# Optimization experiments

Measured on AMD Instinct MI355X. Metric: run time of the kernel, lower is better.

Reference implementation:

```python
import jax, jax.numpy as jnp
import numpy as np

D_MODEL = 1024
NUM_HEADS = 16
HEAD_DIM = D_MODEL // NUM_HEADS


def setup_inputs() -> dict:
    key = jax.random.key(0)
    k1, k2, k3 = jax.random.split(key, 3)
    B, S = 2, 2048
    x = jax.random.normal(k1, (B, S, D_MODEL), dtype=jnp.float32)
    # torch nn.Linear weight layout: [out_features, in_features]
    qkv_w = jax.random.normal(k2, (3 * D_MODEL, D_MODEL), dtype=jnp.float32) * (D_MODEL ** -0.5)
    qkv_b = jnp.zeros((3 * D_MODEL,), dtype=jnp.float32)
    out_w = jax.random.normal(k3, (D_MODEL, D_MODEL), dtype=jnp.float32) * (D_MODEL ** -0.5)
    out_b = jnp.zeros((D_MODEL,), dtype=jnp.float32)
    return {"x": x, "qkv_w": qkv_w, "qkv_b": qkv_b, "out_w": out_w, "out_b": out_b}


def reference(x, qkv_w, qkv_b, out_w, out_b):
    B, S, D = x.shape
    H, hd = NUM_HEADS, HEAD_DIM
    # fused QKV projection (torch Linear: x @ W.T + b)
    qkv = jnp.dot(x, qkv_w.T) + qkv_b              # [B, S, 3D]
    qkv = qkv.reshape(B, S, 3, H, hd)
    qkv = jnp.transpose(qkv, (2, 0, 3, 1, 4))       # [3, B, H, S, hd]
    q, k, v = qkv[0], qkv[1], qkv[2]
    scale = hd ** -0.5
    scores = jnp.einsum('bhqd,bhkd->bhqk', q, k) * scale  # [B, H, S, S]
    # causal mask (TritonSoftmax(is_causal=True))
    causal = jnp.tril(jnp.ones((S, S), dtype=bool))
    scores = jnp.where(causal, scores, jnp.float32(-jnp.inf))
    attn = jax.nn.softmax(scores, axis=-1)
    ctx = jnp.einsum('bhqk,bhkd->bhqd', attn, v)    # [B, H, S, hd]
    ctx = jnp.transpose(ctx, (0, 2, 1, 3)).reshape(B, S, D)
    return jnp.dot(ctx, out_w.T) + out_b
```

## Files before the change

kernel.cpp:

```cpp
#include <hip/hip_runtime.h>

typedef unsigned short u16;
typedef __bf16 bf16x8 __attribute__((ext_vector_type(8)));
typedef float f32x4 __attribute__((ext_vector_type(4)));

#define LOG2E 1.44269504088896340736f

__device__ __forceinline__ u16 f2bf(float f) {
  unsigned int u = __builtin_bit_cast(unsigned int, f);
  u += 0x7FFFu + ((u >> 16) & 1u);
  return (u16)(u >> 16);
}

__device__ __forceinline__ void async16(const void* g, void* l) {
  __builtin_amdgcn_global_load_lds((void*)g, (void*)l, 16, 0, 0);
}

__global__ void cast_f32_bf16(const float* __restrict__ src, u16* __restrict__ dst, int n4) {
  int i = blockIdx.x * blockDim.x + threadIdx.x;
  if (i >= n4) return;
  float4 v = ((const float4*)src)[i];
  union { u16 s[4]; uint2 u; } o;
  o.s[0] = f2bf(v.x); o.s[1] = f2bf(v.y); o.s[2] = f2bf(v.z); o.s[3] = f2bf(v.w);
  ((uint2*)dst)[i] = o.u;
}

template <int EPI>
__global__ __launch_bounds__(256)
void gemm_nt(const u16* __restrict__ A, const u16* __restrict__ Bw,
             int M, int N, int K, const float* __restrict__ bias,
             u16* __restrict__ qo, u16* __restrict__ ko, u16* __restrict__ vto,
             float* __restrict__ out, int ntn) {
  __shared__ __align__(16) u16 As[128 * 32];
  __shared__ __align__(16) u16 Bs[128 * 32];
  const int tid = threadIdx.x;
  const int w = tid >> 6, lane = tid & 63;
  const int lr = lane & 15, lkb = lane >> 4;
  const int bx = blockIdx.x;
  const int mt = bx / ntn, nt = bx % ntn;
  const int m0 = mt * 128, n0 = nt * 128;
  const int wm = (w >> 1) * 64, wn = (w & 1) * 64;

  f32x4 acc[4][4] = {};

  int srow[2], sgch[2];
#pragma unroll
  for (int i = 0; i < 2; ++i) {
    int cid = tid + i * 256;
    srow[i] = cid >> 2;
    sgch[i] = (cid & 3) ^ (srow[i] & 3);
  }

  for (int k0 = 0; k0 < K; k0 += 32) {
#pragma unroll
    for (int i = 0; i < 2; ++i) {
      char* la = (char*)As + (w * 64 + i * 256) * 16;
      async16(A + (size_t)(m0 + srow[i]) * K + k0 + sgch[i] * 8, la);
      char* lb = (char*)Bs + (w * 64 + i * 256) * 16;
      async16(Bw + (size_t)(n0 + srow[i]) * K + k0 + sgch[i] * 8, lb);
    }
    __syncthreads();

    bf16x8 af[4], bfr[4];
#pragma unroll
    for (int i = 0; i < 4; ++i) {
      int ra = wm + i * 16 + lr;
      af[i] = *(const bf16x8*)(As + ra * 32 + (lkb ^ (ra & 3)) * 8);
      int rb = wn + i * 16 + lr;
      bfr[i] = *(const bf16x8*)(Bs + rb * 32 + (lkb ^ (rb & 3)) * 8);
    }
#pragma unroll
    for (int i = 0; i < 4; ++i)
#pragma unroll
      for (int j = 0; j < 4; ++j)
        acc[i][j] = __builtin_amdgcn_mfma_f32_16x16x32_bf16(af[i], bfr[j], acc[i][j], 0, 0, 0);
    __syncthreads();
  }

  if constexpr (EPI == 0) {
    const int which = n0 >> 10;
    const float qscale = (which == 0) ? 0.125f : 1.0f;
#pragma unroll
    for (int i = 0; i < 4; ++i) {
#pragma unroll
      for (int j = 0; j < 4; ++j) {
        int n = n0 + wn + j * 16 + lr;
        float bv = bias[n];
        int d = n & 1023, h = d >> 6, dd = d & 63;
#pragma unroll
        for (int r = 0; r < 4; ++r) {
          int m = m0 + wm + i * 16 + lkb * 4 + r;
          int b = m >> 11, s = m & 2047;
          int bh = b * 16 + h;
          u16 val = f2bf((acc[i][j][r] + bv) * qscale);
          if (which == 0)      qo[(bh * 2048 + s) * 64 + dd] = val;
          else if (which == 1) ko[(bh * 2048 + s) * 64 + dd] = val;
          else                 vto[(bh * 64 + dd) * 2048 + s] = val;
        }
      }
    }
  } else {
#pragma unroll
    for (int i = 0; i < 4; ++i)
#pragma unroll
      for (int j = 0; j < 4; ++j) {
        int n = n0 + wn + j * 16 + lr;
        float bv = bias[n];
#pragma unroll
        for (int r = 0; r < 4; ++r) {
          int m = m0 + wm + i * 16 + lkb * 4 + r;
          out[(size_t)m * N + n] = acc[i][j][r] + bv;
        }
      }
  }
}

__global__ __launch_bounds__(256)
void flash_attn(const u16* __restrict__ Q, const u16* __restrict__ Kg,
                const u16* __restrict__ Vt, u16* __restrict__ ctx) {
  __shared__ __align__(16) u16 Kls[64 * 64];
  __shared__ __align__(16) u16 Vls[64 * 64];
  __shared__ __align__(16) u16 Pls[4][16 * 72];
  const int tid = threadIdx.x;
  const int w = tid >> 6, lane = tid & 63;
  const int lr = lane & 15, lkb = lane >> 4;
  const int bid = blockIdx.x;
  const int qt = 31 - (bid >> 5);
  const int bh = bid & 31;
  const int q0 = qt * 64;
  const u16* Qh = Q + (size_t)bh * 2048 * 64;
  const u16* Kh = Kg + (size_t)bh * 2048 * 64;
  const u16* Vh = Vt + (size_t)bh * 2048 * 64;

  bf16x8 aQ[2];
#pragma unroll
  for (int kk = 0; kk < 2; ++kk)
    aQ[kk] = *(const bf16x8*)(Qh + (q0 + w * 16 + lr) * 64 + lkb * 8 + kk * 32);

  f32x4 acc[4] = {};
  float mrow[4] = {-1e30f, -1e30f, -1e30f, -1e30f};
  float lrow[4] = {0.f, 0.f, 0.f, 0.f};

  int srow[2], sgch[2];
#pragma unroll
  for (int i = 0; i < 2; ++i) {
    int cid = tid + i * 256;
    srow[i] = cid >> 3;
    sgch[i] = (cid & 7) ^ (srow[i] & 7);
  }

  const int nkv = qt + 1;
  for (int t = 0; t < nkv; ++t) {
    const int kv0 = t * 64;
#pragma unroll
    for (int i = 0; i < 2; ++i) {
      char* lk = (char*)Kls + (w * 64 + i * 256) * 16;
      async16(Kh + (size_t)(kv0 + srow[i]) * 64 + sgch[i] * 8, lk);
      char* lv = (char*)Vls + (w * 64 + i * 256) * 16;
      async16(Vh + (size_t)srow[i] * 2048 + kv0 + sgch[i] * 8, lv);
    }
    __syncthreads();

    f32x4 sc[4];
#pragma unroll
    for (int ct = 0; ct < 4; ++ct) {
      int row = ct * 16 + lr;
      int rs = row & 7;
      bf16x8 b0 = *(const bf16x8*)(Kls + row * 64 + (lkb ^ rs) * 8);
      bf16x8 b1 = *(const bf16x8*)(Kls + row * 64 + ((lkb + 4) ^ rs) * 8);
      f32x4 z = {};
      z = __builtin_amdgcn_mfma_f32_16x16x32_bf16(aQ[0], b0, z, 0, 0, 0);
      z = __builtin_amdgcn_mfma_f32_16x16x32_bf16(aQ[1], b1, z, 0, 0, 0);
      sc[ct] = z;
    }

    if (t == qt) {
#pragma unroll
      for (int ct = 0; ct < 4; ++ct) {
        int col = kv0 + ct * 16 + lr;
#pragma unroll
        for (int r = 0; r < 4; ++r) {
          int qr = q0 + w * 16 + lkb * 4 + r;
          if (col > qr) sc[ct][r] = -1e30f;
        }
      }
    }

#pragma unroll
    for (int r = 0; r < 4; ++r) {
      float mt = fmaxf(fmaxf(sc[0][r], sc[1][r]), fmaxf(sc[2][r], sc[3][r]));
      mt = fmaxf(mt, __shfl_xor(mt, 1));
      mt = fmaxf(mt, __shfl_xor(mt, 2));
      mt = fmaxf(mt, __shfl_xor(mt, 4));
      mt = fmaxf(mt, __shfl_xor(mt, 8));
      float mnew = fmaxf(mrow[r], mt);
      float a = exp2f((mrow[r] - mnew) * LOG2E);
      mrow[r] = mnew;
      float rsum = 0.f;
#pragma unroll
      for (int ct = 0; ct < 4; ++ct) {
        float p = exp2f((sc[ct][r] - mnew) * LOG2E);
        sc[ct][r] = p;
        rsum += p;
      }
      rsum += __shfl_xor(rsum, 1);
      rsum += __shfl_xor(rsum, 2);
      rsum += __shfl_xor(rsum, 4);
      rsum += __shfl_xor(rsum, 8);
      lrow[r] = lrow[r] * a + rsum;
#pragma unroll
      for (int dt = 0; dt < 4; ++dt) acc[dt][r] *= a;
    }

    u16* pw = &Pls[w][0];
#pragma unroll
    for (int ct = 0; ct < 4; ++ct)
#pragma unroll
      for (int r = 0; r < 4; ++r)
        pw[(lkb * 4 + r) * 72 + ct * 16 + lr] = f2bf(sc[ct][r]);

    bf16x8 aP0 = *(const bf16x8*)(pw + lr * 72 + lkb * 8);
    bf16x8 aP1 = *(const bf16x8*)(pw + lr * 72 + lkb * 8 + 32);

#pragma unroll
    for (int dt = 0; dt < 4; ++dt) {
      int row = dt * 16 + lr;
      int rs = row & 7;
      bf16x8 v0 = *(const bf16x8*)(Vls + row * 64 + (lkb ^ rs) * 8);
      bf16x8 v1 = *(const bf16x8*)(Vls + row * 64 + ((lkb + 4) ^ rs) * 8);
      acc[dt] = __builtin_amdgcn_mfma_f32_16x16x32_bf16(aP0, v0, acc[dt], 0, 0, 0);
      acc[dt] = __builtin_amdgcn_mfma_f32_16x16x32_bf16(aP1, v1, acc[dt], 0, 0, 0);
    }
    __syncthreads();
  }

  const int b = bh >> 4, h = bh & 15;
#pragma unroll
  for (int r = 0; r < 4; ++r) {
    float rl = 1.0f / lrow[r];
    int qr = q0 + w * 16 + lkb * 4 + r;
    size_t base = ((size_t)(b * 2048 + qr)) * 1024 + h * 64;
#pragma unroll
    for (int dt = 0; dt < 4; ++dt)
      ctx[base + dt * 16 + lr] = f2bf(acc[dt][r] * rl);
  }
}

extern "C" void kernel_launch(void* const* d_in, const int* in_sizes, int n_in,
                              void* d_out, int out_size, void* d_ws, size_t ws_size,
                              hipStream_t stream) {
  (void)in_sizes; (void)n_in; (void)out_size; (void)ws_size;
  const float* x = (const float*)d_in[0];
  const float* qkv_w = (const float*)d_in[1];
  const float* qkv_b = (const float*)d_in[2];
  const float* out_w = (const float*)d_in[3];
  const float* out_b = (const float*)d_in[4];
  float* out = (float*)d_out;

  char* ws = (char*)d_ws;
  u16* xb   = (u16*)(ws);
  u16* wqkv = (u16*)(ws + 8388608);
  u16* wout = (u16*)(ws + 14680064);
  u16* Qb   = (u16*)(ws + 16777216);
  u16* Kb   = (u16*)(ws + 25165824);
  u16* Vtb  = (u16*)(ws + 33554432);
  u16* ctx  = (u16*)(ws + 41943040);

  cast_f32_bf16<<<4096, 256, 0, stream>>>(x, xb, 1048576);
  cast_f32_bf16<<<3072, 256, 0, stream>>>(qkv_w, wqkv, 786432);
  cast_f32_bf16<<<1024, 256, 0, stream>>>(out_w, wout, 262144);

  gemm_nt<0><<<768, 256, 0, stream>>>(xb, wqkv, 4096, 3072, 1024, qkv_b,
                                      Qb, Kb, Vtb, nullptr, 24);
  flash_attn<<<1024, 256, 0, stream>>>(Qb, Kb, Vtb, ctx);
  gemm_nt<1><<<256, 256, 0, stream>>>(ctx, wout, 4096, 1024, 1024, out_b,
                                      nullptr, nullptr, nullptr, out, 8);
}
```

Before: 229.4 us.

## Double-buffer flash attention, shuffle P in registers, fuse casts, retile output GEMM

Flash attention now double-buffers the K/V tiles so the next tile loads while the current one computes. It also transposes the MFMA operands so each lane owns one query row, builds P in registers with cvt_pk and cross-lane shuffles instead of going through LDS, and skips the rescale when the max grows by less than a threshold. The three cast kernels are merged into one launch, and the output GEMM uses 128x64 tiles to double the block count. The cost is more LDS per block and extra shuffle instructions, and the lazy rescale could change numerics if scores grow large.

```diff
diff --git a/kernel.cpp b/kernel.cpp
--- a/kernel.cpp
+++ b/kernel.cpp
@@ -12,36 +12,49 @@
   return (u16)(u >> 16);
 }
 
+__device__ __forceinline__ unsigned int cvtpk_bf16(float lo, float hi) {
+  unsigned int r;
+  asm("v_cvt_pk_bf16_f32 %0, %1, %2" : "=v"(r) : "v"(lo), "v"(hi));
+  return r;
+}
+
 __device__ __forceinline__ void async16(const void* g, void* l) {
   __builtin_amdgcn_global_load_lds((void*)g, (void*)l, 16, 0, 0);
 }
 
-__global__ void cast_f32_bf16(const float* __restrict__ src, u16* __restrict__ dst, int n4) {
+__global__ void cast_all(const float* __restrict__ x, const float* __restrict__ w1,
+                         const float* __restrict__ w2, u16* __restrict__ xb,
+                         u16* __restrict__ w1b, u16* __restrict__ w2b) {
   int i = blockIdx.x * blockDim.x + threadIdx.x;
-  if (i >= n4) return;
-  float4 v = ((const float4*)src)[i];
-  union { u16 s[4]; uint2 u; } o;
-  o.s[0] = f2bf(v.x); o.s[1] = f2bf(v.y); o.s[2] = f2bf(v.z); o.s[3] = f2bf(v.w);
-  ((uint2*)dst)[i] = o.u;
-}
-
-template <int EPI>
+  const float* s; u16* d; int j;
+  if (i < 1048576)      { s = x;  d = xb;  j = i; }
+  else if (i < 1835008) { s = w1; d = w1b; j = i - 1048576; }
+  else                  { s = w2; d = w2b; j = i - 1835008; }
+  float4 v = ((const float4*)s)[j];
+  union { u16 s4[4]; uint2 u; } o;
+  o.s4[0] = f2bf(v.x); o.s4[1] = f2bf(v.y); o.s4[2] = f2bf(v.z); o.s4[3] = f2bf(v.w);
+  ((uint2*)d)[j] = o.u;
+}
+
+template <int EPI, int BN>
 __global__ __launch_bounds__(256)
 void gemm_nt(const u16* __restrict__ A, const u16* __restrict__ Bw,
              int M, int N, int K, const float* __restrict__ bias,
              u16* __restrict__ qo, u16* __restrict__ ko, u16* __restrict__ vto,
              float* __restrict__ out, int ntn) {
   __shared__ __align__(16) u16 As[128 * 32];
-  __shared__ __align__(16) u16 Bs[128 * 32];
+  __shared__ __align__(16) u16 Bs[BN * 32];
+  constexpr int JN = BN / 32;
+  constexpr int NB = (BN * 4) / 256;
   const int tid = threadIdx.x;
   const int w = tid >> 6, lane = tid & 63;
   const int lr = lane & 15, lkb = lane >> 4;
   const int bx = blockIdx.x;
   const int mt = bx / ntn, nt = bx % ntn;
-  const int m0 = mt * 128, n0 = nt * 128;
-  const int wm = (w >> 1) * 64, wn = (w & 1) * 64;
-
-  f32x4 acc[4][4] = {};
+  const int m0 = mt * 128, n0 = nt * BN;
+  const int wm = (w >> 1) * 64, wn = (w & 1) * (BN / 2);
+
+  f32x4 acc[4][JN] = {};
 
   int srow[2], sgch[2];
 #pragma unroll
@@ -56,23 +69,29 @@
     for (int i = 0; i < 2; ++i) {
       char* la = (char*)As + (w * 64 + i * 256) * 16;
       async16(A + (size_t)(m0 + srow[i]) * K + k0 + sgch[i] * 8, la);
+    }
+#pragma unroll
+    for (int i = 0; i < NB; ++i) {
       char* lb = (char*)Bs + (w * 64 + i * 256) * 16;
       async16(Bw + (size_t)(n0 + srow[i]) * K + k0 + sgch[i] * 8, lb);
     }
     __syncthreads();
 
-    bf16x8 af[4], bfr[4];
+    bf16x8 af[4], bfr[JN];
 #pragma unroll
     for (int i = 0; i < 4; ++i) {
       int ra = wm + i * 16 + lr;
       af[i] = *(const bf16x8*)(As + ra * 32 + (lkb ^ (ra & 3)) * 8);
-      int rb = wn + i * 16 + lr;
-      bfr[i] = *(const bf16x8*)(Bs + rb * 32 + (lkb ^ (rb & 3)) * 8);
+    }
+#pragma unroll
+    for (int j = 0; j < JN; ++j) {
+      int rb = wn + j * 16 + lr;
+      bfr[j] = *(const bf16x8*)(Bs + rb * 32 + (lkb ^ (rb & 3)) * 8);
     }
 #pragma unroll
     for (int i = 0; i < 4; ++i)
 #pragma unroll
-      for (int j = 0; j < 4; ++j)
+      for (int j = 0; j < JN; ++j)
         acc[i][j] = __builtin_amdgcn_mfma_f32_16x16x32_bf16(af[i], bfr[j], acc[i][j], 0, 0, 0);
     __syncthreads();
   }
@@ -83,7 +102,7 @@
 #pragma unroll
     for (int i = 0; i < 4; ++i) {
 #pragma unroll
-      for (int j = 0; j < 4; ++j) {
+      for (int j = 0; j < JN; ++j) {
         int n = n0 + wn + j * 16 + lr;
         float bv = bias[n];
         int d = n & 1023, h = d >> 6, dd = d & 63;
@@ -103,7 +122,7 @@
 #pragma unroll
     for (int i = 0; i < 4; ++i)
 #pragma unroll
-      for (int j = 0; j < 4; ++j) {
+      for (int j = 0; j < JN; ++j) {
         int n = n0 + wn + j * 16 + lr;
         float bv = bias[n];
 #pragma unroll
@@ -118,9 +137,8 @@
 __global__ __launch_bounds__(256)
 void flash_attn(const u16* __restrict__ Q, const u16* __restrict__ Kg,
                 const u16* __restrict__ Vt, u16* __restrict__ ctx) {
-  __shared__ __align__(16) u16 Kls[64 * 64];
-  __shared__ __align__(16) u16 Vls[64 * 64];
-  __shared__ __align__(16) u16 Pls[4][16 * 72];
+  __shared__ __align__(16) u16 Kls[2][64 * 64];
+  __shared__ __align__(16) u16 Vls[2][64 * 64];
   const int tid = threadIdx.x;
   const int w = tid >> 6, lane = tid & 63;
   const int lr = lane & 15, lkb = lane >> 4;
@@ -135,11 +153,10 @@
   bf16x8 aQ[2];
 #pragma unroll
   for (int kk = 0; kk < 2; ++kk)
-    aQ[kk] = *(const bf16x8*)(Qh + (q0 + w * 16 + lr) * 64 + lkb * 8 + kk * 32);
+    aQ[kk] = *(const bf16x8*)(Qh + (q0 + w * 16 + lr) * 64 + kk * 32 + lkb * 8);
 
   f32x4 acc[4] = {};
-  float mrow[4] = {-1e30f, -1e30f, -1e30f, -1e30f};
-  float lrow[4] = {0.f, 0.f, 0.f, 0.f};
+  float m_r = -1e30f, l_r = 0.f;
 
   int srow[2], sgch[2];
 #pragma unroll
@@ -150,99 +167,136 @@
   }
 
   const int nkv = qt + 1;
+
+  {
+#pragma unroll
+    for (int i = 0; i < 2; ++i) {
+      char* lk = (char*)&Kls[0][0] + (w * 64 + i * 256) * 16;
+      async16(Kh + (size_t)srow[i] * 64 + sgch[i] * 8, lk);
+      char* lv = (char*)&Vls[0][0] + (w * 64 + i * 256) * 16;
+      async16(Vh + (size_t)srow[i] * 2048 + sgch[i] * 8, lv);
+    }
+  }
+  __syncthreads();
+
   for (int t = 0; t < nkv; ++t) {
-    const int kv0 = t * 64;
-#pragma unroll
-    for (int i = 0; i < 2; ++i) {
-      char* lk = (char*)Kls + (w * 64 + i * 256) * 16;
-      async16(Kh + (size_t)(kv0 + srow[i]) * 64 + sgch[i] * 8, lk);
-      char* lv = (char*)Vls + (w * 64 + i * 256) * 16;
-      async16(Vh + (size_t)srow[i] * 2048 + kv0 + sgch[i] * 8, lv);
-    }
-    __syncthreads();
+    const int cur = t & 1;
+    if (t + 1 < nkv) {
+      const int kv1 = (t + 1) * 64;
+#pragma unroll
+      for (int i = 0; i < 2; ++i) {
+        char* lk = (char*)&Kls[cur ^ 1][0] + (w * 64 + i * 256) * 16;
+        async16(Kh + (size_t)(kv1 + srow[i]) * 64 + sgch[i] * 8, lk);
+        char* lv = (char*)&Vls[cur ^ 1][0] + (w * 64 + i * 256) * 16;
+        async16(Vh + (size_t)srow[i] * 2048 + kv1 + sgch[i] * 8, lv);
+      }
+    }
+    const u16* Kb = &Kls[cur][0];
+    const u16* Vb = &Vls[cur][0];
 
     f32x4 sc[4];
 #pragma unroll
     for (int ct = 0; ct < 4; ++ct) {
       int row = ct * 16 + lr;
       int rs = row & 7;
-      bf16x8 b0 = *(const bf16x8*)(Kls + row * 64 + (lkb ^ rs) * 8);
-      bf16x8 b1 = *(const bf16x8*)(Kls + row * 64 + ((lkb + 4) ^ rs) * 8);
+      bf16x8 k0 = *(const bf16x8*)(Kb + row * 64 + (lkb ^ rs) * 8);
+      bf16x8 k1 = *(const bf16x8*)(Kb + row * 64 + ((lkb + 4) ^ rs) * 8);
       f32x4 z = {};
-      z = __builtin_amdgcn_mfma_f32_16x16x32_bf16(aQ[0], b0, z, 0, 0, 0);
-      z = __builtin_amdgcn_mfma_f32_16x16x32_bf16(aQ[1], b1, z, 0, 0, 0);
+      z = __builtin_amdgcn_mfma_f32_16x16x32_bf16(k0, aQ[0], z, 0, 0, 0);
+      z = __builtin_amdgcn_mfma_f32_16x16x32_bf16(k1, aQ[1], z, 0, 0, 0);
       sc[ct] = z;
     }
 
     if (t == qt) {
 #pragma unroll
-      for (int ct = 0; ct < 4; ++ct) {
-        int col = kv0 + ct * 16 + lr;
-#pragma unroll
-        for (int r = 0; r < 4; ++r) {
-          int qr = q0 + w * 16 + lkb * 4 + r;
-          if (col > qr) sc[ct][r] = -1e30f;
-        }
-      }
-    }
-
-#pragma unroll
-    for (int r = 0; r < 4; ++r) {
-      float mt = fmaxf(fmaxf(sc[0][r], sc[1][r]), fmaxf(sc[2][r], sc[3][r]));
-      mt = fmaxf(mt, __shfl_xor(mt, 1));
-      mt = fmaxf(mt, __shfl_xor(mt, 2));
-      mt = fmaxf(mt, __shfl_xor(mt, 4));
-      mt = fmaxf(mt, __shfl_xor(mt, 8));
-      float mnew = fmaxf(mrow[r], mt);
-      float a = exp2f((mrow[r] - mnew) * LOG2E);
-      mrow[r] = mnew;
-      float rsum = 0.f;
-#pragma unroll
-      for (int ct = 0; ct < 4; ++ct) {
-        float p = exp2f((sc[ct][r] - mnew) * LOG2E);
+      for (int ct = 0; ct < 4; ++ct)
+#pragma unroll
+        for (int r = 0; r < 4; ++r)
+          if (ct * 16 + lkb * 4 + r > w * 16 + lr) sc[ct][r] = -1e30f;
+    }
+
+    float g0 = fmaxf(fmaxf(sc[0][0], sc[0][1]), fmaxf(sc[0][2], sc[0][3]));
+    float g1 = fmaxf(fmaxf(sc[1][0], sc[1][1]), fmaxf(sc[1][2], sc[1][3]));
+    float g2 = fmaxf(fmaxf(sc[2][0], sc[2][1]), fmaxf(sc[2][2], sc[2][3]));
+    float g3 = fmaxf(fmaxf(sc[3][0], sc[3][1]), fmaxf(sc[3][2], sc[3][3]));
+    float mt = fmaxf(fmaxf(g0, g1), fmaxf(g2, g3));
+    mt = fmaxf(mt, __shfl_xor(mt, 16));
+    mt = fmaxf(mt, __shfl_xor(mt, 32));
+
+    if (!__all(mt <= m_r + 8.0f)) {
+      float mnew = fmaxf(m_r, mt);
+      float a = exp2f((m_r - mnew) * LOG2E);
+      l_r *= a;
+#pragma unroll
+      for (int dt = 0; dt < 4; ++dt) acc[dt] *= a;
+      m_r = mnew;
+    }
+    const float mls = m_r * LOG2E;
+    float rsum = 0.f;
+#pragma unroll
+    for (int ct = 0; ct < 4; ++ct)
+#pragma unroll
+      for (int r = 0; r < 4; ++r) {
+        float p = exp2f(__builtin_fmaf(sc[ct][r], LOG2E, -mls));
         sc[ct][r] = p;
         rsum += p;
       }
-      rsum += __shfl_xor(rsum, 1);
-      rsum += __shfl_xor(rsum, 2);
-      rsum += __shfl_xor(rsum, 4);
-      rsum += __shfl_xor(rsum, 8);
-      lrow[r] = lrow[r] * a + rsum;
-#pragma unroll
-      for (int dt = 0; dt < 4; ++dt) acc[dt][r] *= a;
-    }
-
-    u16* pw = &Pls[w][0];
-#pragma unroll
-    for (int ct = 0; ct < 4; ++ct)
-#pragma unroll
-      for (int r = 0; r < 4; ++r)
-        pw[(lkb * 4 + r) * 72 + ct * 16 + lr] = f2bf(sc[ct][r]);
-
-    bf16x8 aP0 = *(const bf16x8*)(pw + lr * 72 + lkb * 8);
-    bf16x8 aP1 = *(const bf16x8*)(pw + lr * 72 + lkb * 8 + 32);
+    rsum += __shfl_xor(rsum, 16);
+    rsum += __shfl_xor(rsum, 32);
+    l_r += rsum;
+
+    unsigned int u[4][2];
+#pragma unroll
+    for (int ct = 0; ct < 4; ++ct) {
+      u[ct][0] = cvtpk_bf16(sc[ct][0], sc[ct][1]);
+      u[ct][1] = cvtpk_bf16(sc[ct][2], sc[ct][3]);
+    }
+
+    const int s0 = ((lkb & 1) << 5) + lr;
+    const int s1 = s0 + 16;
+    const int hi = lkb >> 1;
+    bf16x8 Pf[2];
+#pragma unroll
+    for (int c = 0; c < 2; ++c) {
+      const int c2 = c * 2;
+      unsigned x0 = (unsigned)__shfl((int)u[c2][0], s0, 64);
+      unsigned x1 = (unsigned)__shfl((int)u[c2][1], s0, 64);
+      unsigned x2 = (unsigned)__shfl((int)u[c2][0], s1, 64);
+      unsigned x3 = (unsigned)__shfl((int)u[c2][1], s1, 64);
+      unsigned y0 = (unsigned)__shfl((int)u[c2 + 1][0], s0, 64);
+      unsigned y1 = (unsigned)__shfl((int)u[c2 + 1][1], s0, 64);
+      unsigned y2 = (unsigned)__shfl((int)u[c2 + 1][0], s1, 64);
+      unsigned y3 = (unsigned)__shfl((int)u[c2 + 1][1], s1, 64);
+      uint4 bb;
+      bb.x = hi ? y0 : x0;
+      bb.y = hi ? y1 : x1;
+      bb.z = hi ? y2 : x2;
+      bb.w = hi ? y3 : x3;
+      Pf[c] = __builtin_bit_cast(bf16x8, bb);
+    }
 
 #pragma unroll
     for (int dt = 0; dt < 4; ++dt) {
       int row = dt * 16 + lr;
       int rs = row & 7;
-      bf16x8 v0 = *(const bf16x8*)(Vls + row * 64 + (lkb ^ rs) * 8);
-      bf16x8 v1 = *(const bf16x8*)(Vls + row * 64 + ((lkb + 4) ^ rs) * 8);
-      acc[dt] = __builtin_amdgcn_mfma_f32_16x16x32_bf16(aP0, v0, acc[dt], 0, 0, 0);
-      acc[dt] = __builtin_amdgcn_mfma_f32_16x16x32_bf16(aP1, v1, acc[dt], 0, 0, 0);
+      bf16x8 v0 = *(const bf16x8*)(Vb + row * 64 + (lkb ^ rs) * 8);
+      bf16x8 v1 = *(const bf16x8*)(Vb + row * 64 + ((lkb + 4) ^ rs) * 8);
+      acc[dt] = __builtin_amdgcn_mfma_f32_16x16x32_bf16(v0, Pf[0], acc[dt], 0, 0, 0);
+      acc[dt] = __builtin_amdgcn_mfma_f32_16x16x32_bf16(v1, Pf[1], acc[dt], 0, 0, 0);
     }
     __syncthreads();
   }
 
+  const float rl = 1.0f / l_r;
   const int b = bh >> 4, h = bh & 15;
-#pragma unroll
-  for (int r = 0; r < 4; ++r) {
-    float rl = 1.0f / lrow[r];
-    int qr = q0 + w * 16 + lkb * 4 + r;
-    size_t base = ((size_t)(b * 2048 + qr)) * 1024 + h * 64;
-#pragma unroll
-    for (int dt = 0; dt < 4; ++dt)
-      ctx[base + dt * 16 + lr] = f2bf(acc[dt][r] * rl);
+  const int q = q0 + w * 16 + lr;
+  const size_t base = ((size_t)(b * 2048 + q)) * 1024 + h * 64;
+#pragma unroll
+  for (int dt = 0; dt < 4; ++dt) {
+    uint2 o;
+    o.x = cvtpk_bf16(acc[dt][0] * rl, acc[dt][1] * rl);
+    o.y = cvtpk_bf16(acc[dt][2] * rl, acc[dt][3] * rl);
+    *(uint2*)(ctx + base + dt * 16 + lkb * 4) = o;
   }
 }
 
@@ -266,13 +320,11 @@
   u16* Vtb  = (u16*)(ws + 33554432);
   u16* ctx  = (u16*)(ws + 41943040);
 
-  cast_f32_bf16<<<4096, 256, 0, stream>>>(x, xb, 1048576);
-  cast_f32_bf16<<<3072, 256, 0, stream>>>(qkv_w, wqkv, 786432);
-  cast_f32_bf16<<<1024, 256, 0, stream>>>(out_w, wout, 262144);
-
-  gemm_nt<0><<<768, 256, 0, stream>>>(xb, wqkv, 4096, 3072, 1024, qkv_b,
-                                      Qb, Kb, Vtb, nullptr, 24);
+  cast_all<<<8192, 256, 0, stream>>>(x, qkv_w, out_w, xb, wqkv, wout);
+
+  gemm_nt<0, 128><<<768, 256, 0, stream>>>(xb, wqkv, 4096, 3072, 1024, qkv_b,
+                                           Qb, Kb, Vtb, nullptr, 24);
   flash_attn<<<1024, 256, 0, stream>>>(Qb, Kb, Vtb, ctx);
-  gemm_nt<1><<<256, 256, 0, stream>>>(ctx, wout, 4096, 1024, 1024, out_b,
-                                      nullptr, nullptr, nullptr, out, 8);
-}
+  gemm_nt<1, 64><<<512, 256, 0, stream>>>(ctx, wout, 4096, 1024, 1024, out_b,
+                                          nullptr, nullptr, nullptr, out, 16);
+}
```

New measurement: 200.7 us. 1.14x faster.
